# Kernel tuning notes

Measured on AMD Instinct MI355X. Metric: run time of the kernel, lower is better.

The kernel has to match this reference:

```python
import jax, jax.numpy as jnp
import numpy as np

G = 8        # n_games
D_IN = 128   # per-game state dim
A = 16       # per-game action dim
H1 = 600     # n_hidden_1
H2 = 500     # n_hidden_2
B = 32768    # batch


def setup_inputs() -> dict:
    key = jax.random.key(0)
    ks = jax.random.split(key, 12)
    u = lambda k, shape, bound: jax.random.uniform(k, shape, jnp.float32, -bound, bound)
    state = jax.random.normal(ks[0], (B, D_IN), jnp.float32)
    action = jax.random.normal(ks[1], (B, A), jnp.float32)
    idx = jnp.sort(jax.random.randint(ks[2], (B,), 0, G)).astype(jnp.int32)
    inp = {
        "state": state,
        "action": action,
        "idx": idx,
        # per-game first layer: Linear(D_IN -> H1), uniform(-1/sqrt(fan_in))
        "W1": u(ks[3], (G, H1, D_IN), 1.0 / np.sqrt(D_IN)),
        "b1": u(ks[4], (G, H1), 1.0 / np.sqrt(D_IN)),
        # shared state layer: Linear(H1 -> H2)
        "W2s": u(ks[5], (H2, H1), 1.0 / np.sqrt(H1)),
        "b2s": u(ks[6], (H2,), 1.0 / np.sqrt(H1)),
        # per-game action layer: Linear(A -> H2, bias=False)
        "W2a": u(ks[7], (G, H2, A), 1.0 / np.sqrt(A)),
        # per-game output head: Linear(H2 -> 1), uniform(-0.003, 0.003)
        "W3": u(ks[8], (G, H2), 0.003),
        "b3": u(ks[9], (G,), 0.003),
    }
    return inp


def reference(state, action, idx, W1, b1, W2s, b2s, W2a, W3, b3):
    # Per-game h1 for all games, then pick the routed game per sample.
    # (Reference-clean equivalent of the Python loop over unique idx; idx is
    #  sorted so the original's group reordering is the identity.)
    h1_all = jax.nn.relu(jnp.einsum('bd,ghd->bgh', state, W1) + b1)      # [B,G,H1]
    h1 = jnp.take_along_axis(h1_all, idx[:, None, None], axis=1)[:, 0]  # [B,H1]

    h2a_all = jnp.einsum('ba,gha->bgh', action, W2a)                     # [B,G,H2]
    h2a = jnp.take_along_axis(h2a_all, idx[:, None, None], axis=1)[:, 0]

    h2 = jnp.einsum('bh,kh->bk', h1, W2s) + b2s + h2a                    # [B,H2]
    h_f = jax.nn.relu(h2)  # features == 'relu'

    q_all = jnp.einsum('bh,gh->bg', h_f, W3) + b3                        # [B,G]
    q = jnp.take_along_axis(q_all, idx[:, None], axis=1)[:, 0]           # [B]
    return q
```

## Files before the change

### kernel.cpp

```cpp
#include <hip/hip_runtime.h>

#define G_ 8
#define DIN 128
#define ACT 16
#define H1 600
#define H2 500
#define H1P 608
#define H2P 512
#define BT 128
#define NB 256
#define NCHUNK 19
#define NTHR 512

#define OFF_W2S 0
#define OFF_W1  622592
#define OFF_W2A 1867776
#define OFF_B1  1998848
#define OFF_B2S 2018304
#define OFF_W3  2020352

#define LDS_STATE 0u
#define LDS_W2S   32768u
#define LDS_H1    98304u
#define LDS_W1    114688u
#define LDS_IDX   131072u
#define LDS_TOTAL 131584

typedef __attribute__((ext_vector_type(8))) short short8;
typedef __attribute__((ext_vector_type(4))) float f32x4;
typedef __attribute__((ext_vector_type(16))) float f32x16;

__device__ __forceinline__ unsigned short f2bf(float f) {
  unsigned u = __float_as_uint(f);
  unsigned r = u + 0x7fffu + ((u >> 16) & 1u);
  return (unsigned short)(r >> 16);
}

__device__ __forceinline__ short8 pack8(const float* v) {
  short8 p;
#pragma unroll
  for (int j = 0; j < 8; ++j) p[j] = (short)f2bf(v[j]);
  return p;
}

__device__ __forceinline__ void stage1k(unsigned lds_off, const void* g) {
  __builtin_amdgcn_global_load_lds(
      (const __attribute__((address_space(1))) unsigned int*)(unsigned long long)g,
      (__attribute__((address_space(3))) unsigned int*)lds_off,
      16, 0, 0);
}

__device__ __forceinline__ void stage_w2s(const char* ws, int chunk, int buf, int w, int lane) {
  const char* src = ws + OFF_W2S + (size_t)chunk * 32768;
#pragma unroll
  for (int u = 0; u < 4; ++u) {
    const int unit = w * 4 + u;
    stage1k(LDS_W2S + (unsigned)(buf * 32768 + unit * 1024), src + unit * 1024 + lane * 16);
  }
}

__device__ __forceinline__ void stage_w1(const char* ws, int g, int chunk, int buf, int w, int lane) {
  const char* src = ws + OFF_W1 + ((size_t)g * NCHUNK + chunk) * 8192;
  stage1k(LDS_W1 + (unsigned)(buf * 8192 + w * 1024), src + w * 1024 + lane * 16);
}

__global__ __launch_bounds__(256) void prep_kernel(
    const float* __restrict__ W1, const float* __restrict__ b1,
    const float* __restrict__ W2s, const float* __restrict__ b2s,
    const float* __restrict__ W2a, const float* __restrict__ W3,
    char* __restrict__ ws)
{
  unsigned short* w2s_img = (unsigned short*)(ws + OFF_W2S);
  unsigned short* w1_img  = (unsigned short*)(ws + OFF_W1);
  unsigned short* w2a_img = (unsigned short*)(ws + OFF_W2A);
  float* b1p  = (float*)(ws + OFF_B1);
  float* b2sp = (float*)(ws + OFF_B2S);
  float* w3p  = (float*)(ws + OFF_W3);
  const int tid = blockIdx.x * blockDim.x + threadIdx.x;
  const int nthr = gridDim.x * blockDim.x;

  for (int e = tid; e < 311296; e += nthr) {
    int chunk = e >> 14;
    int t  = (e >> 13) & 1;
    int ct = (e >> 9) & 15;
    int l  = (e >> 3) & 63;
    int j  = e & 7;
    int c = ct * 32 + (l & 31);
    int k = chunk * 32 + t * 16 + ((l >> 5) << 3) + j;
    float v = (c < H2 && k < H1) ? W2s[c * H1 + k] : 0.f;
    w2s_img[e] = f2bf(v);
  }
  for (int e = tid; e < 622592; e += nthr) {
    int g = e / 77824;
    int rem = e - g * 77824;
    int chunk = rem >> 12;
    int rem2 = rem & 4095;
    int ks = rem2 >> 10;
    int ft = (rem2 >> 9) & 1;
    int l  = (rem2 >> 3) & 63;
    int j  = rem2 & 7;
    int f = chunk * 32 + ft * 16 + (l & 15);
    int d = ks * 32 + ((l >> 4) << 3) + j;
    float v = (f < H1) ? W1[((size_t)g * H1 + f) * DIN + d] : 0.f;
    w1_img[e] = f2bf(v);
  }
  for (int e = tid; e < 65536; e += nthr) {
    int g = e >> 13;
    int rem = e & 8191;
    int ct = rem >> 9;
    int l  = (rem >> 3) & 63;
    int j  = rem & 7;
    int c = ct * 32 + (l & 31);
    int a = ((l >> 5) << 3) + j;
    float v = (c < H2) ? W2a[((size_t)g * H2 + c) * ACT + a] : 0.f;
    w2a_img[e] = f2bf(v);
  }
  for (int e = tid; e < G_ * H1P; e += nthr) {
    int g = e / H1P, f = e - g * H1P;
    b1p[e] = (f < H1) ? b1[g * H1 + f] : 0.f;
  }
  for (int e = tid; e < H2P; e += nthr)
    b2sp[e] = (e < H2) ? b2s[e] : 0.f;
  for (int e = tid; e < G_ * H2P; e += nthr) {
    int g = e >> 9, c = e & 511;
    w3p[e] = (c < H2) ? W3[g * H2 + c] : 0.f;
  }
}

__global__ __launch_bounds__(NTHR, 2) void critic_main(
    const float* __restrict__ state, const float* __restrict__ action,
    const int* __restrict__ idx, const float* __restrict__ b3,
    const char* __restrict__ ws, float* __restrict__ out)
{
  extern __shared__ char smem[];
  const int tid  = threadIdx.x;
  const int lane = tid & 63;
  const int w    = tid >> 6;
  const int s0   = blockIdx.x * BT;
  int* idx_lds = (int*)(smem + LDS_IDX);

  const unsigned short* w1img  = (const unsigned short*)(ws + OFF_W1);
  const unsigned short* w2aimg = (const unsigned short*)(ws + OFF_W2A);
  const float* b1p  = (const float*)(ws + OFF_B1);
  const float* b2sp = (const float*)(ws + OFF_B2S);
  const float* w3p  = (const float*)(ws + OFF_W3);

  if (tid < BT) idx_lds[tid] = idx[s0 + tid];
  {
    const int row = tid >> 2;
    const int cg  = tid & 3;
    const float* sp = state + (size_t)(s0 + row) * DIN + cg * 32;
    float v[32];
#pragma unroll
    for (int u = 0; u < 8; ++u) {
      f32x4 t4 = *(const f32x4*)(sp + u * 4);
      v[u*4+0] = t4[0]; v[u*4+1] = t4[1]; v[u*4+2] = t4[2]; v[u*4+3] = t4[3];
    }
#pragma unroll
    for (int u = 0; u < 4; ++u) {
      short8 p = pack8(v + u * 8);
      const int lslot = u * 16 + (row & 15);
      const unsigned off = LDS_STATE + (unsigned)((((row >> 4) * 4 + cg) * 64 + lslot) * 16);
      *(short8*)(smem + off) = p;
    }
  }
  __syncthreads();

  const int g_lo = idx_lds[0];
  const int g_hi = idx_lds[BT - 1];

  stage_w2s(ws, 0, 0, w, lane);
  stage_w1(ws, g_lo, 0, 0, w, lane);
  stage_w1(ws, g_lo, 1, 1, w, lane);

  f32x16 acc2[2][4];
#pragma unroll
  for (int a = 0; a < 2; ++a)
#pragma unroll
    for (int n = 0; n < 4; ++n)
#pragma unroll
      for (int r = 0; r < 16; ++r) acc2[a][n][r] = 0.f;
  {
    short8 bact[4];
#pragma unroll
    for (int nt = 0; nt < 4; ++nt) {
      const float* ap = action + (size_t)(s0 + nt * 32 + (lane & 31)) * ACT + ((lane >> 5) << 3);
      float av[8];
      f32x4 a0 = *(const f32x4*)ap, a1 = *(const f32x4*)(ap + 4);
      av[0]=a0[0];av[1]=a0[1];av[2]=a0[2];av[3]=a0[3];
      av[4]=a1[0];av[5]=a1[1];av[6]=a1[2];av[7]=a1[3];
      bact[nt] = pack8(av);
    }
    for (int g = g_lo; g <= g_hi; ++g) {
#pragma unroll
      for (int cti = 0; cti < 2; ++cti) {
        const int ct = w * 2 + cti;
        short8 af = *(const short8*)(w2aimg + (((size_t)g * 16 + ct) * 64 + lane) * 8);
#pragma unroll
        for (int nt = 0; nt < 4; ++nt) {
          f32x16 z;
#pragma unroll
          for (int r = 0; r < 16; ++r) z[r] = 0.f;
          f32x16 t = __builtin_amdgcn_mfma_f32_32x32x16_bf16(af, bact[nt], z, 0, 0, 0);
          const bool p = (idx_lds[nt * 32 + (lane & 31)] == g);
#pragma unroll
          for (int r = 0; r < 16; ++r) acc2[cti][nt][r] = p ? t[r] : acc2[cti][nt][r];
        }
      }
    }
  }

  asm volatile("s_waitcnt vmcnt(0)" ::: "memory");
  __syncthreads();

  auto layer1 = [&](int c, int buf) {
    for (int g = g_lo; g <= g_hi; ++g) {
      f32x4 a1acc[2];
#pragma unroll
      for (int ft = 0; ft < 2; ++ft) { a1acc[ft][0]=0.f;a1acc[ft][1]=0.f;a1acc[ft][2]=0.f;a1acc[ft][3]=0.f; }
#pragma unroll
      for (int ks = 0; ks < 4; ++ks) {
        short8 bs = *(const short8*)(smem + LDS_STATE + (unsigned)(((w * 4 + ks) * 64 + lane) * 16));
#pragma unroll
        for (int ft = 0; ft < 2; ++ft) {
          short8 aw;
          if (g == g_lo)
            aw = *(const short8*)(smem + LDS_W1 + (unsigned)(buf * 8192 + (ks * 2 + ft) * 1024 + lane * 16));
          else
            aw = *(const short8*)(w1img + (((size_t)g * NCHUNK + c) * 8 + ks * 2 + ft) * 512 + lane * 8);
          a1acc[ft] = __builtin_amdgcn_mfma_f32_16x16x32_bf16(aw, bs, a1acc[ft], 0, 0, 0);
        }
      }
      const int sl = w * 16 + (lane & 15);
      if (idx_lds[sl] == g) {
        const int kloc  = (lane >> 4) << 2;
        const int khalf = kloc >> 3;
        const int j0    = kloc & 7;
        const int s32   = (w & 1) * 16 + (lane & 15);
        const int nt    = w >> 1;
#pragma unroll
        for (int ft = 0; ft < 2; ++ft) {
          const int fglob = c * 32 + ft * 16 + kloc;
          unsigned long long pkv = 0ull;
#pragma unroll
          for (int r = 0; r < 4; ++r) {
            float hv = a1acc[ft][r] + b1p[g * H1P + fglob + r];
            hv = fmaxf(hv, 0.f);
            pkv |= ((unsigned long long)f2bf(hv)) << (16 * r);
          }
          const unsigned off = LDS_H1 + (unsigned)(buf * 8192 + ft * 4096 + nt * 1024 + (khalf * 32 + s32) * 16 + j0 * 2);
          *(unsigned long long*)(smem + off) = pkv;
        }
      }
    }
  };

  layer1(0, 0);
  __syncthreads();

  for (int i = 0; i < NCHUNK; ++i) {
    const int cur = i & 1, nxt = cur ^ 1;
    if (i + 1 < NCHUNK) stage_w2s(ws, i + 1, nxt, w, lane);
    if (i + 2 < NCHUNK) stage_w1(ws, g_lo, i + 2, cur, w, lane);

#pragma unroll
    for (int t = 0; t < 2; ++t) {
      short8 bf[4];
#pragma unroll
      for (int nt = 0; nt < 4; ++nt)
        bf[nt] = *(const short8*)(smem + LDS_H1 + (unsigned)(cur * 8192 + t * 4096 + nt * 1024 + lane * 16));
#pragma unroll
      for (int cti = 0; cti < 2; ++cti) {
        short8 af = *(const short8*)(smem + LDS_W2S + (unsigned)(cur * 32768 + t * 16384 + (w * 2 + cti) * 1024 + lane * 16));
#pragma unroll
        for (int nt = 0; nt < 4; ++nt)
          acc2[cti][nt] = __builtin_amdgcn_mfma_f32_32x32x16_bf16(af, bf[nt], acc2[cti][nt], 0, 0, 0);
      }
    }

    if (i + 1 < NCHUNK) layer1(i + 1, nxt);
    asm volatile("s_waitcnt vmcnt(0)" ::: "memory");
    __syncthreads();
  }

  float qp[4] = {0.f, 0.f, 0.f, 0.f};
#pragma unroll
  for (int cti = 0; cti < 2; ++cti) {
    const int ctbase = (w * 2 + cti) * 32 + ((lane >> 5) << 2);
#pragma unroll
    for (int r = 0; r < 16; ++r) {
      const int c = ctbase + (r & 3) + ((r >> 2) << 3);
      const float b2v = b2sp[c];
#pragma unroll
      for (int nt = 0; nt < 4; ++nt) {
        const int gs = idx_lds[nt * 32 + (lane & 31)];
        float v2 = acc2[cti][nt][r] + b2v;
        v2 = fmaxf(v2, 0.f);
        qp[nt] += v2 * w3p[gs * H2P + c];
      }
    }
  }
#pragma unroll
  for (int nt = 0; nt < 4; ++nt) {
    float v2 = qp[nt];
    v2 += __shfl_xor(v2, 32, 64);
    if (lane < 32) {
      const int sl = nt * 32 + lane;
      float add = v2;
      if (w == 0) add += b3[idx_lds[sl]];
      atomicAdd(out + s0 + sl, add);
    }
  }
}

extern "C" void kernel_launch(void* const* d_in, const int* in_sizes, int n_in,
                              void* d_out, int out_size, void* d_ws, size_t ws_size,
                              hipStream_t stream) {
  const float* state  = (const float*)d_in[0];
  const float* action = (const float*)d_in[1];
  const int*   idx    = (const int*)d_in[2];
  const float* W1     = (const float*)d_in[3];
  const float* b1     = (const float*)d_in[4];
  const float* W2s    = (const float*)d_in[5];
  const float* b2s    = (const float*)d_in[6];
  const float* W2a    = (const float*)d_in[7];
  const float* W3     = (const float*)d_in[8];
  const float* b3     = (const float*)d_in[9];
  float* out = (float*)d_out;
  char* ws = (char*)d_ws;

  (void)hipFuncSetAttribute((const void*)critic_main,
                            hipFuncAttributeMaxDynamicSharedMemorySize, LDS_TOTAL);
  hipMemsetAsync(d_out, 0, 32768 * sizeof(float), stream);
  hipLaunchKernelGGL(prep_kernel, dim3(1024), dim3(256), 0, stream,
                     W1, b1, W2s, b2s, W2a, W3, ws);
  hipLaunchKernelGGL(critic_main, dim3(NB), dim3(NTHR), LDS_TOTAL, stream,
                     state, action, idx, b3, ws, out);
}
```

Baseline: 131.9 us.

## Split output columns across two blocks, read W2s from global, shrink LDS

Each 128-sample tile is now handled by two blocks, each computing half of the H2 output columns. The W2s staging in LDS is dropped in favour of direct global reads, and state fragments stay in registers, so LDS use falls from about 128KB to 33KB and launch bounds allow four blocks per CU. The prep kernel is vectorised to handle eight elements per thread and runs on fewer blocks. The trade-off is that layer-1 work is duplicated across the two half-blocks, W2s is fetched from L2 with no LDS reuse, and the layer-2 MMA section is given raised wave priority.

```diff
diff --git a/kernel.cpp b/kernel.cpp
--- a/kernel.cpp
+++ b/kernel.cpp
@@ -8,7 +8,7 @@
 #define H1P 608
 #define H2P 512
 #define BT 128
-#define NB 256
+#define NBLK 512
 #define NCHUNK 19
 #define NTHR 512
 
@@ -19,12 +19,10 @@
 #define OFF_B2S 2018304
 #define OFF_W3  2020352
 
-#define LDS_STATE 0u
-#define LDS_W2S   32768u
-#define LDS_H1    98304u
-#define LDS_W1    114688u
-#define LDS_IDX   131072u
-#define LDS_TOTAL 131584
+#define LDS_H1  0u
+#define LDS_W1  16384u
+#define LDS_IDX 32768u
+#define LDS_TOTAL 33280
 
 typedef __attribute__((ext_vector_type(8))) short short8;
 typedef __attribute__((ext_vector_type(4))) float f32x4;
@@ -48,20 +46,6 @@
       (const __attribute__((address_space(1))) unsigned int*)(unsigned long long)g,
       (__attribute__((address_space(3))) unsigned int*)lds_off,
       16, 0, 0);
-}
-
-__device__ __forceinline__ void stage_w2s(const char* ws, int chunk, int buf, int w, int lane) {
-  const char* src = ws + OFF_W2S + (size_t)chunk * 32768;
-#pragma unroll
-  for (int u = 0; u < 4; ++u) {
-    const int unit = w * 4 + u;
-    stage1k(LDS_W2S + (unsigned)(buf * 32768 + unit * 1024), src + unit * 1024 + lane * 16);
-  }
-}
-
-__device__ __forceinline__ void stage_w1(const char* ws, int g, int chunk, int buf, int w, int lane) {
-  const char* src = ws + OFF_W1 + ((size_t)g * NCHUNK + chunk) * 8192;
-  stage1k(LDS_W1 + (unsigned)(buf * 8192 + w * 1024), src + w * 1024 + lane * 16);
 }
 
 __global__ __launch_bounds__(256) void prep_kernel(
@@ -70,50 +54,67 @@
     const float* __restrict__ W2a, const float* __restrict__ W3,
     char* __restrict__ ws)
 {
-  unsigned short* w2s_img = (unsigned short*)(ws + OFF_W2S);
-  unsigned short* w1_img  = (unsigned short*)(ws + OFF_W1);
-  unsigned short* w2a_img = (unsigned short*)(ws + OFF_W2A);
+  short8* w2s_img = (short8*)(ws + OFF_W2S);
+  short8* w1_img  = (short8*)(ws + OFF_W1);
+  short8* w2a_img = (short8*)(ws + OFF_W2A);
   float* b1p  = (float*)(ws + OFF_B1);
   float* b2sp = (float*)(ws + OFF_B2S);
   float* w3p  = (float*)(ws + OFF_W3);
   const int tid = blockIdx.x * blockDim.x + threadIdx.x;
   const int nthr = gridDim.x * blockDim.x;
 
-  for (int e = tid; e < 311296; e += nthr) {
-    int chunk = e >> 14;
-    int t  = (e >> 13) & 1;
-    int ct = (e >> 9) & 15;
-    int l  = (e >> 3) & 63;
-    int j  = e & 7;
-    int c = ct * 32 + (l & 31);
-    int k = chunk * 32 + t * 16 + ((l >> 5) << 3) + j;
-    float v = (c < H2 && k < H1) ? W2s[c * H1 + k] : 0.f;
-    w2s_img[e] = f2bf(v);
-  }
-  for (int e = tid; e < 622592; e += nthr) {
-    int g = e / 77824;
-    int rem = e - g * 77824;
-    int chunk = rem >> 12;
-    int rem2 = rem & 4095;
-    int ks = rem2 >> 10;
-    int ft = (rem2 >> 9) & 1;
-    int l  = (rem2 >> 3) & 63;
-    int j  = rem2 & 7;
-    int f = chunk * 32 + ft * 16 + (l & 15);
-    int d = ks * 32 + ((l >> 4) << 3) + j;
-    float v = (f < H1) ? W1[((size_t)g * H1 + f) * DIN + d] : 0.f;
-    w1_img[e] = f2bf(v);
-  }
-  for (int e = tid; e < 65536; e += nthr) {
-    int g = e >> 13;
-    int rem = e & 8191;
-    int ct = rem >> 9;
-    int l  = (rem >> 3) & 63;
-    int j  = rem & 7;
-    int c = ct * 32 + (l & 31);
-    int a = ((l >> 5) << 3) + j;
-    float v = (c < H2) ? W2a[((size_t)g * H2 + c) * ACT + a] : 0.f;
-    w2a_img[e] = f2bf(v);
+  for (int u = tid; u < 38912; u += nthr) {
+    const int e0 = u << 3;
+    const int chunk = e0 >> 14, t = (e0 >> 13) & 1, ct = (e0 >> 9) & 15, l = (e0 >> 3) & 63;
+    const int cc = ct * 32 + (l & 31);
+    const int k0 = chunk * 32 + t * 16 + ((l >> 5) << 3);
+    float v[8];
+    if (cc < H2 && k0 < H1) {
+      const float* p = W2s + (size_t)cc * H1 + k0;
+      f32x4 a0 = *(const f32x4*)p, a1 = *(const f32x4*)(p + 4);
+      v[0]=a0[0];v[1]=a0[1];v[2]=a0[2];v[3]=a0[3];
+      v[4]=a1[0];v[5]=a1[1];v[6]=a1[2];v[7]=a1[3];
+    } else {
+#pragma unroll
+      for (int j = 0; j < 8; ++j) v[j] = 0.f;
+    }
+    w2s_img[u] = pack8(v);
+  }
+  for (int u = tid; u < 77824; u += nthr) {
+    const int g = u / 9728;
+    const int rem = u - g * 9728;
+    const int chunk = rem >> 9;
+    const int rem2 = rem & 511;
+    const int ks = rem2 >> 7, ft = (rem2 >> 6) & 1, l = rem2 & 63;
+    const int f = chunk * 32 + ft * 16 + (l & 15);
+    const int d0 = ks * 32 + ((l >> 4) << 3);
+    float v[8];
+    if (f < H1) {
+      const float* p = W1 + ((size_t)g * H1 + f) * DIN + d0;
+      f32x4 a0 = *(const f32x4*)p, a1 = *(const f32x4*)(p + 4);
+      v[0]=a0[0];v[1]=a0[1];v[2]=a0[2];v[3]=a0[3];
+      v[4]=a1[0];v[5]=a1[1];v[6]=a1[2];v[7]=a1[3];
+    } else {
+#pragma unroll
+      for (int j = 0; j < 8; ++j) v[j] = 0.f;
+    }
+    w1_img[u] = pack8(v);
+  }
+  for (int u = tid; u < 8192; u += nthr) {
+    const int g = u >> 10, ct = (u >> 6) & 15, l = u & 63;
+    const int cc = ct * 32 + (l & 31);
+    const int a0 = (l >> 5) << 3;
+    float v[8];
+    if (cc < H2) {
+      const float* p = W2a + ((size_t)g * H2 + cc) * ACT + a0;
+      f32x4 x0 = *(const f32x4*)p, x1 = *(const f32x4*)(p + 4);
+      v[0]=x0[0];v[1]=x0[1];v[2]=x0[2];v[3]=x0[3];
+      v[4]=x1[0];v[5]=x1[1];v[6]=x1[2];v[7]=x1[3];
+    } else {
+#pragma unroll
+      for (int j = 0; j < 8; ++j) v[j] = 0.f;
+    }
+    w2a_img[u] = pack8(v);
   }
   for (int e = tid; e < G_ * H1P; e += nthr) {
     int g = e / H1P, f = e - g * H1P;
@@ -127,7 +128,7 @@
   }
 }
 
-__global__ __launch_bounds__(NTHR, 2) void critic_main(
+__global__ __launch_bounds__(NTHR, 4) void critic_main(
     const float* __restrict__ state, const float* __restrict__ action,
     const int* __restrict__ idx, const float* __restrict__ b3,
     const char* __restrict__ ws, float* __restrict__ out)
@@ -136,9 +137,13 @@
   const int tid  = threadIdx.x;
   const int lane = tid & 63;
   const int w    = tid >> 6;
-  const int s0   = blockIdx.x * BT;
+  const int h    = blockIdx.x & 1;
+  const int s0   = (blockIdx.x >> 1) * BT;
+  const int cp   = w & 3;
+  const int np   = w >> 2;
   int* idx_lds = (int*)(smem + LDS_IDX);
 
+  const unsigned short* w2simg = (const unsigned short*)(ws + OFF_W2S);
   const unsigned short* w1img  = (const unsigned short*)(ws + OFF_W1);
   const unsigned short* w2aimg = (const unsigned short*)(ws + OFF_W2A);
   const float* b1p  = (const float*)(ws + OFF_B1);
@@ -146,66 +151,62 @@
   const float* w3p  = (const float*)(ws + OFF_W3);
 
   if (tid < BT) idx_lds[tid] = idx[s0 + tid];
+
+  short8 bs[4];
   {
-    const int row = tid >> 2;
-    const int cg  = tid & 3;
-    const float* sp = state + (size_t)(s0 + row) * DIN + cg * 32;
-    float v[32];
-#pragma unroll
-    for (int u = 0; u < 8; ++u) {
-      f32x4 t4 = *(const f32x4*)(sp + u * 4);
-      v[u*4+0] = t4[0]; v[u*4+1] = t4[1]; v[u*4+2] = t4[2]; v[u*4+3] = t4[3];
-    }
-#pragma unroll
-    for (int u = 0; u < 4; ++u) {
-      short8 p = pack8(v + u * 8);
-      const int lslot = u * 16 + (row & 15);
-      const unsigned off = LDS_STATE + (unsigned)((((row >> 4) * 4 + cg) * 64 + lslot) * 16);
-      *(short8*)(smem + off) = p;
-    }
+    const float* sp = state + (size_t)(s0 + w * 16 + (lane & 15)) * DIN + ((lane >> 4) << 3);
+#pragma unroll
+    for (int ks = 0; ks < 4; ++ks) {
+      float v[8];
+      f32x4 t0 = *(const f32x4*)(sp + ks * 32);
+      f32x4 t1 = *(const f32x4*)(sp + ks * 32 + 4);
+      v[0]=t0[0];v[1]=t0[1];v[2]=t0[2];v[3]=t0[3];
+      v[4]=t1[0];v[5]=t1[1];v[6]=t1[2];v[7]=t1[3];
+      bs[ks] = pack8(v);
+    }
+  }
+  short8 bact[2];
+#pragma unroll
+  for (int nti = 0; nti < 2; ++nti) {
+    const int nt = 2 * np + nti;
+    const float* ap = action + (size_t)(s0 + nt * 32 + (lane & 31)) * ACT + ((lane >> 5) << 3);
+    float v[8];
+    f32x4 a0 = *(const f32x4*)ap, a1 = *(const f32x4*)(ap + 4);
+    v[0]=a0[0];v[1]=a0[1];v[2]=a0[2];v[3]=a0[3];
+    v[4]=a1[0];v[5]=a1[1];v[6]=a1[2];v[7]=a1[3];
+    bact[nti] = pack8(v);
   }
   __syncthreads();
 
   const int g_lo = idx_lds[0];
   const int g_hi = idx_lds[BT - 1];
 
-  stage_w2s(ws, 0, 0, w, lane);
-  stage_w1(ws, g_lo, 0, 0, w, lane);
-  stage_w1(ws, g_lo, 1, 1, w, lane);
-
-  f32x16 acc2[2][4];
+  stage1k(LDS_W1 + (unsigned)(tid * 16),
+          ws + OFF_W1 + ((size_t)(g_lo * NCHUNK + 0)) * 8192 + tid * 16);
+  stage1k(LDS_W1 + (unsigned)(8192 + tid * 16),
+          ws + OFF_W1 + ((size_t)(g_lo * NCHUNK + 1)) * 8192 + tid * 16);
+
+  f32x16 acc[2][2];
 #pragma unroll
   for (int a = 0; a < 2; ++a)
 #pragma unroll
-    for (int n = 0; n < 4; ++n)
-#pragma unroll
-      for (int r = 0; r < 16; ++r) acc2[a][n][r] = 0.f;
-  {
-    short8 bact[4];
-#pragma unroll
-    for (int nt = 0; nt < 4; ++nt) {
-      const float* ap = action + (size_t)(s0 + nt * 32 + (lane & 31)) * ACT + ((lane >> 5) << 3);
-      float av[8];
-      f32x4 a0 = *(const f32x4*)ap, a1 = *(const f32x4*)(ap + 4);
-      av[0]=a0[0];av[1]=a0[1];av[2]=a0[2];av[3]=a0[3];
-      av[4]=a1[0];av[5]=a1[1];av[6]=a1[2];av[7]=a1[3];
-      bact[nt] = pack8(av);
-    }
-    for (int g = g_lo; g <= g_hi; ++g) {
-#pragma unroll
-      for (int cti = 0; cti < 2; ++cti) {
-        const int ct = w * 2 + cti;
-        short8 af = *(const short8*)(w2aimg + (((size_t)g * 16 + ct) * 64 + lane) * 8);
-#pragma unroll
-        for (int nt = 0; nt < 4; ++nt) {
-          f32x16 z;
-#pragma unroll
-          for (int r = 0; r < 16; ++r) z[r] = 0.f;
-          f32x16 t = __builtin_amdgcn_mfma_f32_32x32x16_bf16(af, bact[nt], z, 0, 0, 0);
-          const bool p = (idx_lds[nt * 32 + (lane & 31)] == g);
-#pragma unroll
-          for (int r = 0; r < 16; ++r) acc2[cti][nt][r] = p ? t[r] : acc2[cti][nt][r];
-        }
+    for (int n = 0; n < 2; ++n)
+#pragma unroll
+      for (int r = 0; r < 16; ++r) acc[a][n][r] = 0.f;
+  for (int g = g_lo; g <= g_hi; ++g) {
+#pragma unroll
+    for (int cti = 0; cti < 2; ++cti) {
+      const int ctg = h * 8 + cp * 2 + cti;
+      short8 af = *(const short8*)(w2aimg + (((size_t)g * 16 + ctg) * 64 + lane) * 8);
+#pragma unroll
+      for (int nti = 0; nti < 2; ++nti) {
+        f32x16 z;
+#pragma unroll
+        for (int r = 0; r < 16; ++r) z[r] = 0.f;
+        f32x16 t = __builtin_amdgcn_mfma_f32_32x32x16_bf16(af, bact[nti], z, 0, 0, 0);
+        const bool p = (idx_lds[(2 * np + nti) * 32 + (lane & 31)] == g);
+#pragma unroll
+        for (int r = 0; r < 16; ++r) acc[cti][nti][r] = p ? t[r] : acc[cti][nti][r];
       }
     }
   }
@@ -220,7 +221,6 @@
       for (int ft = 0; ft < 2; ++ft) { a1acc[ft][0]=0.f;a1acc[ft][1]=0.f;a1acc[ft][2]=0.f;a1acc[ft][3]=0.f; }
 #pragma unroll
       for (int ks = 0; ks < 4; ++ks) {
-        short8 bs = *(const short8*)(smem + LDS_STATE + (unsigned)(((w * 4 + ks) * 64 + lane) * 16));
 #pragma unroll
         for (int ft = 0; ft < 2; ++ft) {
           short8 aw;
@@ -228,27 +228,26 @@
             aw = *(const short8*)(smem + LDS_W1 + (unsigned)(buf * 8192 + (ks * 2 + ft) * 1024 + lane * 16));
           else
             aw = *(const short8*)(w1img + (((size_t)g * NCHUNK + c) * 8 + ks * 2 + ft) * 512 + lane * 8);
-          a1acc[ft] = __builtin_amdgcn_mfma_f32_16x16x32_bf16(aw, bs, a1acc[ft], 0, 0, 0);
+          a1acc[ft] = __builtin_amdgcn_mfma_f32_16x16x32_bf16(aw, bs[ks], a1acc[ft], 0, 0, 0);
         }
       }
       const int sl = w * 16 + (lane & 15);
       if (idx_lds[sl] == g) {
         const int kloc  = (lane >> 4) << 2;
-        const int khalf = kloc >> 3;
+        const int khalf = lane >> 5;
         const int j0    = kloc & 7;
+        const int nt    = w >> 1;
         const int s32   = (w & 1) * 16 + (lane & 15);
-        const int nt    = w >> 1;
 #pragma unroll
         for (int ft = 0; ft < 2; ++ft) {
           const int fglob = c * 32 + ft * 16 + kloc;
           unsigned long long pkv = 0ull;
 #pragma unroll
           for (int r = 0; r < 4; ++r) {
-            float hv = a1acc[ft][r] + b1p[g * H1P + fglob + r];
-            hv = fmaxf(hv, 0.f);
+            float hv = fmaxf(a1acc[ft][r] + b1p[g * H1P + fglob + r], 0.f);
             pkv |= ((unsigned long long)f2bf(hv)) << (16 * r);
           }
-          const unsigned off = LDS_H1 + (unsigned)(buf * 8192 + ft * 4096 + nt * 1024 + (khalf * 32 + s32) * 16 + j0 * 2);
+          const unsigned off = LDS_H1 + (unsigned)(buf * 8192 + (ft * 4 + nt) * 1024 + (khalf * 32 + s32) * 16 + j0 * 2);
           *(unsigned long long*)(smem + off) = pkv;
         }
       }
@@ -260,55 +259,56 @@
 
   for (int i = 0; i < NCHUNK; ++i) {
     const int cur = i & 1, nxt = cur ^ 1;
-    if (i + 1 < NCHUNK) stage_w2s(ws, i + 1, nxt, w, lane);
-    if (i + 2 < NCHUNK) stage_w1(ws, g_lo, i + 2, cur, w, lane);
-
+    if (i + 2 < NCHUNK)
+      stage1k(LDS_W1 + (unsigned)(cur * 8192 + tid * 16),
+              ws + OFF_W1 + ((size_t)(g_lo * NCHUNK + i + 2)) * 8192 + tid * 16);
+
+    __builtin_amdgcn_s_setprio(1);
 #pragma unroll
     for (int t = 0; t < 2; ++t) {
-      short8 bf[4];
-#pragma unroll
-      for (int nt = 0; nt < 4; ++nt)
-        bf[nt] = *(const short8*)(smem + LDS_H1 + (unsigned)(cur * 8192 + t * 4096 + nt * 1024 + lane * 16));
-#pragma unroll
-      for (int cti = 0; cti < 2; ++cti) {
-        short8 af = *(const short8*)(smem + LDS_W2S + (unsigned)(cur * 32768 + t * 16384 + (w * 2 + cti) * 1024 + lane * 16));
-#pragma unroll
-        for (int nt = 0; nt < 4; ++nt)
-          acc2[cti][nt] = __builtin_amdgcn_mfma_f32_32x32x16_bf16(af, bf[nt], acc2[cti][nt], 0, 0, 0);
-      }
-    }
+      short8 bf0 = *(const short8*)(smem + LDS_H1 + (unsigned)(cur * 8192 + (t * 4 + 2 * np) * 1024 + lane * 16));
+      short8 bf1 = *(const short8*)(smem + LDS_H1 + (unsigned)(cur * 8192 + (t * 4 + 2 * np + 1) * 1024 + lane * 16));
+      const unsigned short* abase = w2simg + (((size_t)((i * 2 + t) * 16 + h * 8 + cp * 2)) * 64 + lane) * 8;
+      short8 af0 = *(const short8*)(abase);
+      short8 af1 = *(const short8*)(abase + 512);
+      acc[0][0] = __builtin_amdgcn_mfma_f32_32x32x16_bf16(af0, bf0, acc[0][0], 0, 0, 0);
+      acc[0][1] = __builtin_amdgcn_mfma_f32_32x32x16_bf16(af0, bf1, acc[0][1], 0, 0, 0);
+      acc[1][0] = __builtin_amdgcn_mfma_f32_32x32x16_bf16(af1, bf0, acc[1][0], 0, 0, 0);
+      acc[1][1] = __builtin_amdgcn_mfma_f32_32x32x16_bf16(af1, bf1, acc[1][1], 0, 0, 0);
+    }
+    __builtin_amdgcn_s_setprio(0);
 
     if (i + 1 < NCHUNK) layer1(i + 1, nxt);
     asm volatile("s_waitcnt vmcnt(0)" ::: "memory");
     __syncthreads();
   }
 
-  float qp[4] = {0.f, 0.f, 0.f, 0.f};
+  float qp[2] = {0.f, 0.f};
+  int gs[2];
+#pragma unroll
+  for (int nti = 0; nti < 2; ++nti) gs[nti] = idx_lds[(2 * np + nti) * 32 + (lane & 31)];
 #pragma unroll
   for (int cti = 0; cti < 2; ++cti) {
-    const int ctbase = (w * 2 + cti) * 32 + ((lane >> 5) << 2);
+    const int cbase = h * 256 + (cp * 2 + cti) * 32 + ((lane >> 5) << 2);
 #pragma unroll
     for (int r = 0; r < 16; ++r) {
-      const int c = ctbase + (r & 3) + ((r >> 2) << 3);
+      const int c = cbase + (r & 3) + ((r >> 2) << 3);
       const float b2v = b2sp[c];
 #pragma unroll
-      for (int nt = 0; nt < 4; ++nt) {
-        const int gs = idx_lds[nt * 32 + (lane & 31)];
-        float v2 = acc2[cti][nt][r] + b2v;
-        v2 = fmaxf(v2, 0.f);
-        qp[nt] += v2 * w3p[gs * H2P + c];
+      for (int nti = 0; nti < 2; ++nti) {
+        float v2 = fmaxf(acc[cti][nti][r] + b2v, 0.f);
+        qp[nti] += v2 * w3p[gs[nti] * H2P + c];
       }
     }
   }
 #pragma unroll
-  for (int nt = 0; nt < 4; ++nt) {
-    float v2 = qp[nt];
-    v2 += __shfl_xor(v2, 32, 64);
+  for (int nti = 0; nti < 2; ++nti) {
+    float v = qp[nti];
+    v += __shfl_xor(v, 32, 64);
     if (lane < 32) {
-      const int sl = nt * 32 + lane;
-      float add = v2;
-      if (w == 0) add += b3[idx_lds[sl]];
-      atomicAdd(out + s0 + sl, add);
+      const int sl = (2 * np + nti) * 32 + lane;
+      if (h == 0 && cp == 0) v += b3[idx_lds[sl]];
+      atomicAdd(out + s0 + sl, v);
     }
   }
 }
@@ -329,11 +329,9 @@
   float* out = (float*)d_out;
   char* ws = (char*)d_ws;
 
-  (void)hipFuncSetAttribute((const void*)critic_main,
-                            hipFuncAttributeMaxDynamicSharedMemorySize, LDS_TOTAL);
   hipMemsetAsync(d_out, 0, 32768 * sizeof(float), stream);
-  hipLaunchKernelGGL(prep_kernel, dim3(1024), dim3(256), 0, stream,
+  hipLaunchKernelGGL(prep_kernel, dim3(256), dim3(256), 0, stream,
                      W1, b1, W2s, b2s, W2a, W3, ws);
-  hipLaunchKernelGGL(critic_main, dim3(NB), dim3(NTHR), LDS_TOTAL, stream,
+  hipLaunchKernelGGL(critic_main, dim3(NBLK), dim3(NTHR), LDS_TOTAL, stream,
                      state, action, idx, b3, ws, out);
 }
```

Result: slower. 148.4 us (+12.5%).
